# Kernel optimization log

Measured on AMD Instinct MI355X. Metric: run time of the kernel, lower is better.

The kernel has to match this reference:

```python
import jax, jax.numpy as jnp
import numpy as np

N = 6144      # total atoms
F = 128       # hidden_dim
NB = 48       # number of molecules (batch segments)
LONG_RANGE_SCALE = 1.0


def setup_inputs() -> dict:
    key = jax.random.key(0)
    ks = jax.random.split(key, 16)
    s = 1.0 / np.sqrt(F)
    return {
        "h0": jax.random.normal(ks[0], (N, F), jnp.float32),
        "h1": jax.random.normal(ks[1], (N, 3, F), jnp.float32),
        "pos": jax.random.normal(ks[2], (N, 3), jnp.float32),
        "batch": jnp.sort(jax.random.randint(ks[3], (N,), 0, NB)),
        "qW1": jax.random.normal(ks[4], (F, F // 2), jnp.float32) * s,
        "qb1": jnp.zeros((F // 2,), jnp.float32),
        "qW2": jax.random.normal(ks[5], (F // 2, 1), jnp.float32) * s,
        "qb2": jnp.zeros((1,), jnp.float32),
        "cW1": jax.random.normal(ks[6], (F, F // 2), jnp.float32) * s,
        "cb1": jnp.zeros((F // 2,), jnp.float32),
        "cW2": jax.random.normal(ks[7], (F // 2, 1), jnp.float32) * s,
        "cb2": jnp.zeros((1,), jnp.float32),
        "muW": jax.random.normal(ks[8], (F, 1), jnp.float32) * s,
    }


def reference(h0, h1, pos, batch, qW1, qb1, qW2, qb2, cW1, cb1, cW2, cb2, muW):
    n = pos.shape[0]
    # pairwise geometry
    batch_mask = batch[:, None] == batch[None, :]                 # (N,N) bool
    diff = pos[:, None, :] - pos[None, :, :]                      # (N,N,3)
    dist_sq = jnp.sum(diff * diff, axis=-1)                       # (N,N)
    dist = jnp.sqrt(dist_sq + 1e-8)
    valid = batch_mask & ~jnp.eye(n, dtype=bool)
    validf = valid.astype(dist.dtype)

    energy = jnp.zeros((), dist.dtype)

    # --- Coulomb (use_charge) ---
    q = jax.nn.silu(h0 @ qW1 + qb1) @ qW2 + qb2                   # (N,1)
    q_sum = jax.ops.segment_sum(q, batch, num_segments=NB)        # (NB,1)
    cnt = jax.ops.segment_sum(jnp.ones((n, 1), q.dtype), batch, num_segments=NB)
    q_mean = q_sum / jnp.maximum(cnt, 1.0)                        # scatter_mean
    q = q - q_mean[batch]                                         # per-molecule neutrality
    qq = q @ q.T                                                  # (N,N)
    f_taper = 1.0 - jnp.exp(-0.5 * dist)
    E_coul = jnp.sum(qq / dist * f_taper * validf)
    energy = energy + 0.5 * E_coul * 14.399

    # --- van der Waals (use_vdw) ---
    c6 = jax.nn.softplus(jax.nn.silu(h0 @ cW1 + cb1) @ cW2 + cb2)  # (N,1), >0
    c6_ij = jnp.sqrt(c6 @ c6.T)                                    # (N,N)
    r6 = dist_sq ** 3
    E_vdw = -jnp.sum(c6_ij / (r6 + 20.0) * validf)
    energy = energy + 0.5 * E_vdw

    # --- dipole-dipole (use_dipole) ---
    mu = (h1 @ muW)[..., 0]                                        # (N,3)
    mu_dot_mu = mu @ mu.T                                          # (N,N)
    n_ij = diff / (dist[..., None] + 1e-8)                         # (N,N,3)
    mu_dot_n_i = jnp.einsum("id,ijd->ij", mu, n_ij)
    mu_dot_n_j = jnp.einsum("jd,ijd->ij", mu, n_ij)
    inv_r3 = 1.0 / (dist_sq * dist + 10.0)
    E_dip = jnp.sum((mu_dot_mu - 3.0 * mu_dot_n_i * mu_dot_n_j) * inv_r3 * validf)
    energy = energy + 0.5 * E_dip

    return energy * LONG_RANGE_SCALE
```

## Files before the change

### kernel.cpp

```cpp
#include <hip/hip_runtime.h>
#include <math.h>

#define F 128
#define H 64
#define HH 32
#define AT 64
#define NBMOL 48
#define CAP 256
#define SPLIT 16

__device__ __forceinline__ float silu_f(float x) {
    return x / (1.0f + __expf(-x));
}
__device__ __forceinline__ float softplus_f(float x) {
    return fmaxf(x, 0.0f) + log1pf(__expf(-fabsf(x)));
}
__device__ __forceinline__ float frcp(float x) {
    return __builtin_amdgcn_rcpf(x);
}
__device__ __forceinline__ float dot4(float4 a, float4 b) {
    return fmaf(a.x, b.x, fmaf(a.y, b.y, fmaf(a.z, b.z, a.w * b.w)));
}

__global__ __launch_bounds__(256, 4) void k_atom(
    const float* __restrict__ h0, const float* __restrict__ h1,
    const int* __restrict__ batch,
    const float* __restrict__ qW1, const float* __restrict__ qb1,
    const float* __restrict__ qW2,
    const float* __restrict__ cW1, const float* __restrict__ cb1,
    const float* __restrict__ cW2,
    const float* __restrict__ muW,
    float* __restrict__ part,
    float* __restrict__ mu,
    int* __restrict__ segstart, int* __restrict__ segend,
    float* __restrict__ out, int N, int nmlp, int ndip)
{
    __shared__ float4 sW4[HH * 32];
    __shared__ float4 sX4[AT * 32];
    __shared__ float red[4][AT];

    const int b = blockIdx.x;
    const int tid = threadIdx.x;

    if (b < nmlp) {
        const int tile  = b >> 2;
        const int net   = b & 1;
        const int hhalf = (b >> 1) & 1;
        const float* __restrict__ W1 = net ? cW1 : qW1;
        const float* __restrict__ b1 = net ? cb1 : qb1;
        const float* __restrict__ W2 = net ? cW2 : qW2;

        for (int idx = tid; idx < HH * F; idx += 256) {
            int f = idx >> 5;
            int hh = idx & 31;
            float val = W1[f * H + hhalf * HH + hh];
            int f4 = f >> 2, fi = f & 3;
            ((float*)&sW4[hh * 32 + (f4 ^ ((hh >> 1) & 7))])[fi] = val;
        }
        const float4* __restrict__ h0v = (const float4*)h0;
        for (int idx = tid; idx < AT * 32; idx += 256) {
            int a = idx >> 5, f4 = idx & 31;
            int row = min(tile * AT + a, N - 1);
            sX4[a * 32 + (f4 ^ ((a >> 2) & 7))] = h0v[(size_t)row * 32 + f4];
        }
        __syncthreads();

        const int ag = tid & 15;
        const int hg = tid >> 4;
        const int swx = ag & 7;
        const int sww = hg & 7;
        const int h0i = hhalf * HH + 2 * hg;

        float z[4][2];
        {
            float b0 = b1[h0i], b1v = b1[h0i + 1];
            #pragma unroll
            for (int j = 0; j < 4; ++j) { z[j][0] = b0; z[j][1] = b1v; }
        }

        #pragma unroll 4
        for (int f4 = 0; f4 < 32; ++f4) {
            float4 w0 = sW4[(2 * hg) * 32 + (f4 ^ sww)];
            float4 w1 = sW4[(2 * hg + 1) * 32 + (f4 ^ sww)];
            #pragma unroll
            for (int j = 0; j < 4; ++j) {
                float4 x = sX4[(4 * ag + j) * 32 + (f4 ^ swx)];
                z[j][0] += dot4(x, w0);
                z[j][1] += dot4(x, w1);
            }
        }

        const float w2a = W2[h0i], w2b = W2[h0i + 1];
        float p[4];
        #pragma unroll
        for (int j = 0; j < 4; ++j)
            p[j] = fmaf(silu_f(z[j][0]), w2a, silu_f(z[j][1]) * w2b);

        #pragma unroll
        for (int j = 0; j < 4; ++j) {
            p[j] += __shfl_xor(p[j], 16);
            p[j] += __shfl_xor(p[j], 32);
        }
        const int wv = tid >> 6, lane = tid & 63;
        if (lane < 16) {
            #pragma unroll
            for (int j = 0; j < 4; ++j) red[wv][4 * lane + j] = p[j];
        }
        __syncthreads();
        if (tid < AT) {
            float s = red[0][tid] + red[1][tid] + red[2][tid] + red[3][tid];
            int atom = tile * AT + tid;
            if (atom < N) part[(size_t)(net * 2 + hhalf) * N + atom] = s;
        }
    } else if (b < nmlp + ndip) {
        const int slot = tid >> 4;
        const int l = tid & 15;
        int row = (b - nmlp) * 16 + slot;
        if (row < 3 * N) {
            const float4* rp = (const float4*)(h1 + (size_t)row * F);
            const float4* mp = (const float4*)muW;
            float pm = dot4(rp[2 * l], mp[2 * l]) +
                       dot4(rp[2 * l + 1], mp[2 * l + 1]);
            #pragma unroll
            for (int off = 1; off < 16; off <<= 1) pm += __shfl_xor(pm, off);
            if (l == 0) mu[row] = pm;
        }
    } else {
        if (tid == 0) out[0] = 0.0f;
        for (int i = tid; i < N; i += 256) {
            int bb = batch[i];
            if (i == 0 || batch[i - 1] != bb) segstart[bb] = i;
            if (i == N - 1 || batch[i + 1] != bb) segend[bb] = i + 1;
        }
    }
}

__global__ __launch_bounds__(256) void k_pair(
    const float* __restrict__ pos,
    const float* __restrict__ part,
    const float* __restrict__ mu,
    const float* __restrict__ qb2, const float* __restrict__ cb2,
    const int* __restrict__ segstart, const int* __restrict__ segend,
    float* __restrict__ out, int N)
{
    const int b = blockIdx.x;
    const int s = blockIdx.y;
    const int tid = threadIdx.x;
    const int st = segstart[b];
    const int n = segend[b] - st;

    const float* __restrict__ p0 = part;
    const float* __restrict__ p1 = part + N;
    const float* __restrict__ p2 = part + 2 * (size_t)N;
    const float* __restrict__ p3 = part + 3 * (size_t)N;
    const float qb2v = qb2[0], cb2v = cb2[0];

    __shared__ float sq[CAP], sc[CAP], sp[3 * CAP], sm[3 * CAP];
    __shared__ float red[4];

    float e_c = 0.f, e_v = 0.f, e_d = 0.f;

    if (n > 1 && n <= CAP) {
        float partsum = 0.f;
        for (int k = tid; k < n; k += 256) {
            float qv = p0[st + k] + p1[st + k] + qb2v;
            sq[k] = qv; partsum += qv;
            sc[k] = sqrtf(softplus_f(p2[st + k] + p3[st + k] + cb2v));
        }
        for (int k = tid; k < 3 * n; k += 256) {
            sp[k] = pos[3 * st + k];
            sm[k] = mu[3 * st + k];
        }
        #pragma unroll
        for (int off = 32; off > 0; off >>= 1)
            partsum += __shfl_xor(partsum, off);
        if ((tid & 63) == 0) red[tid >> 6] = partsum;
        __syncthreads();
        const float mean = (red[0] + red[1] + red[2] + red[3]) / (float)n;

        const int r = tid >> 4;
        const int c = tid & 15;
        for (int il = s + SPLIT * r; il < n; il += SPLIT * 16) {
            const float qi = sq[il] - mean;
            const float sci = sc[il];
            const float xi = sp[3 * il], yi = sp[3 * il + 1], zi = sp[3 * il + 2];
            const float mxi = sm[3 * il], myi = sm[3 * il + 1], mzi = sm[3 * il + 2];
            for (int jl = c; jl < n; jl += 16) {
                if (jl == il) continue;
                float dx = xi - sp[3 * jl], dy = yi - sp[3 * jl + 1],
                      dz = zi - sp[3 * jl + 2];
                float ds0 = fmaf(dx, dx, fmaf(dy, dy, dz * dz));
                float d = sqrtf(ds0 + 1e-8f);
                float inv_d = frcp(d);
                float qj = sq[jl] - mean;
                e_c = fmaf(qi * qj * inv_d, 1.0f - __expf(-0.5f * d), e_c);
                float r6 = ds0 * ds0 * ds0;
                e_v = fmaf(sci * sc[jl], frcp(r6 + 20.0f), e_v);
                float smx = sm[3 * jl], smy = sm[3 * jl + 1], smz = sm[3 * jl + 2];
                float mdm = fmaf(mxi, smx, fmaf(myi, smy, mzi * smz));
                float mdni = fmaf(mxi, dx, fmaf(myi, dy, mzi * dz)) * inv_d;
                float mdnj = fmaf(smx, dx, fmaf(smy, dy, smz * dz)) * inv_d;
                e_d = fmaf(mdm - 3.0f * mdni * mdnj,
                           frcp(fmaf(ds0, d, 10.0f)), e_d);
            }
        }
    } else if (n > CAP) {
        float partsum = 0.f;
        for (int k = tid; k < n; k += 256)
            partsum += p0[st + k] + p1[st + k] + qb2v;
        #pragma unroll
        for (int off = 32; off > 0; off >>= 1)
            partsum += __shfl_xor(partsum, off);
        if ((tid & 63) == 0) red[tid >> 6] = partsum;
        __syncthreads();
        const float mean = (red[0] + red[1] + red[2] + red[3]) / (float)n;
        const int r = tid >> 4, c = tid & 15;
        for (int j0 = 0; j0 < n; j0 += CAP) {
            const int chunk = min(CAP, n - j0);
            __syncthreads();
            for (int k = tid; k < chunk; k += 256) {
                int j = st + j0 + k;
                sq[k] = p0[j] + p1[j] + qb2v;
                sc[k] = sqrtf(softplus_f(p2[j] + p3[j] + cb2v));
            }
            for (int k = tid; k < 3 * chunk; k += 256) {
                sp[k] = pos[3 * (st + j0) + k];
                sm[k] = mu[3 * (st + j0) + k];
            }
            __syncthreads();
            for (int il = s + SPLIT * r; il < n; il += SPLIT * 16) {
                const int i = st + il;
                const float qi = p0[i] + p1[i] + qb2v - mean;
                const float sci = sqrtf(softplus_f(p2[i] + p3[i] + cb2v));
                const float xi = pos[i * 3], yi = pos[i * 3 + 1], zi = pos[i * 3 + 2];
                const float mxi = mu[i * 3], myi = mu[i * 3 + 1], mzi = mu[i * 3 + 2];
                for (int jl = c; jl < chunk; jl += 16) {
                    if (j0 + jl == il) continue;
                    float dx = xi - sp[3 * jl], dy = yi - sp[3 * jl + 1],
                          dz = zi - sp[3 * jl + 2];
                    float ds0 = fmaf(dx, dx, fmaf(dy, dy, dz * dz));
                    float d = sqrtf(ds0 + 1e-8f);
                    float inv_d = frcp(d);
                    float qj = sq[jl] - mean;
                    e_c = fmaf(qi * qj * inv_d, 1.0f - __expf(-0.5f * d), e_c);
                    float r6 = ds0 * ds0 * ds0;
                    e_v = fmaf(sci * sc[jl], frcp(r6 + 20.0f), e_v);
                    float smx = sm[3 * jl], smy = sm[3 * jl + 1], smz = sm[3 * jl + 2];
                    float mdm = fmaf(mxi, smx, fmaf(myi, smy, mzi * smz));
                    float mdni = fmaf(mxi, dx, fmaf(myi, dy, mzi * dz)) * inv_d;
                    float mdnj = fmaf(smx, dx, fmaf(smy, dy, smz * dz)) * inv_d;
                    e_d = fmaf(mdm - 3.0f * mdni * mdnj,
                               frcp(fmaf(ds0, d, 10.0f)), e_d);
                }
            }
        }
    }

    float vv = fmaf(7.1995f, e_c, fmaf(-0.5f, e_v, 0.5f * e_d));
    #pragma unroll
    for (int off = 32; off > 0; off >>= 1) vv += __shfl_xor(vv, off);
    __syncthreads();
    if ((tid & 63) == 0) red[tid >> 6] = vv;
    __syncthreads();
    if (tid == 0) atomicAdd(out, red[0] + red[1] + red[2] + red[3]);
}

extern "C" void kernel_launch(void* const* d_in, const int* in_sizes, int n_in,
                              void* d_out, int out_size, void* d_ws, size_t ws_size,
                              hipStream_t stream) {
    const float* h0  = (const float*)d_in[0];
    const float* h1  = (const float*)d_in[1];
    const float* pos = (const float*)d_in[2];
    const int*   batch = (const int*)d_in[3];
    const float* qW1 = (const float*)d_in[4];
    const float* qb1 = (const float*)d_in[5];
    const float* qW2 = (const float*)d_in[6];
    const float* qb2 = (const float*)d_in[7];
    const float* cW1 = (const float*)d_in[8];
    const float* cb1 = (const float*)d_in[9];
    const float* cW2 = (const float*)d_in[10];
    const float* cb2 = (const float*)d_in[11];
    const float* muW = (const float*)d_in[12];
    float* out = (float*)d_out;
    const int N = in_sizes[0] / F;

    float* ws = (float*)d_ws;
    int* segstart = (int*)ws;
    int* segend   = (int*)(ws + 48);
    float* part = ws + 128;
    float* mu   = part + 4 * (size_t)N;

    const int ntile = (N + AT - 1) / AT;
    const int nmlp = 4 * ntile;
    const int ndip = (3 * N + 15) / 16;
    const int grid = nmlp + ndip + 1;

    k_atom<<<grid, 256, 0, stream>>>(h0, h1, batch, qW1, qb1, qW2,
                                     cW1, cb1, cW2, muW,
                                     part, mu, segstart, segend, out,
                                     N, nmlp, ndip);
    k_pair<<<dim3(NBMOL, SPLIT), 256, 0, stream>>>(pos, part, mu, qb2, cb2,
                                                   segstart, segend, out, N);
}
```

Measured before the change: 112.5 us.

## Compute full hidden width per MLP block and fuse charge/C6 epilogue into atom kernel

Result: no change. 111.9 us (-0.5%).

```diff
diff --git a/kernel.cpp b/kernel.cpp
--- a/kernel.cpp
+++ b/kernel.cpp
@@ -3,8 +3,7 @@
 
 #define F 128
 #define H 64
-#define HH 32
-#define AT 64
+#define ATILE 32
 #define NBMOL 48
 #define CAP 256
 #define SPLIT 16
@@ -26,62 +25,61 @@
     const float* __restrict__ h0, const float* __restrict__ h1,
     const int* __restrict__ batch,
     const float* __restrict__ qW1, const float* __restrict__ qb1,
-    const float* __restrict__ qW2,
+    const float* __restrict__ qW2, const float* __restrict__ qb2,
     const float* __restrict__ cW1, const float* __restrict__ cb1,
-    const float* __restrict__ cW2,
+    const float* __restrict__ cW2, const float* __restrict__ cb2,
     const float* __restrict__ muW,
-    float* __restrict__ part,
+    float* __restrict__ qout,
+    float* __restrict__ sqc6,
     float* __restrict__ mu,
     int* __restrict__ segstart, int* __restrict__ segend,
     float* __restrict__ out, int N, int nmlp, int ndip)
 {
-    __shared__ float4 sW4[HH * 32];
-    __shared__ float4 sX4[AT * 32];
-    __shared__ float red[4][AT];
+    __shared__ float4 sW4[H * 32];
+    __shared__ float4 sX4[ATILE * 32];
+    __shared__ float red[4][ATILE];
 
     const int b = blockIdx.x;
     const int tid = threadIdx.x;
 
     if (b < nmlp) {
-        const int tile  = b >> 2;
-        const int net   = b & 1;
-        const int hhalf = (b >> 1) & 1;
+        const int tile = b >> 1;
+        const int net  = b & 1;
         const float* __restrict__ W1 = net ? cW1 : qW1;
         const float* __restrict__ b1 = net ? cb1 : qb1;
         const float* __restrict__ W2 = net ? cW2 : qW2;
 
-        for (int idx = tid; idx < HH * F; idx += 256) {
-            int f = idx >> 5;
-            int hh = idx & 31;
-            float val = W1[f * H + hhalf * HH + hh];
+        for (int idx = tid; idx < H * F; idx += 256) {
+            int f = idx >> 6, h = idx & 63;
+            float val = W1[idx];
             int f4 = f >> 2, fi = f & 3;
-            ((float*)&sW4[hh * 32 + (f4 ^ ((hh >> 1) & 7))])[fi] = val;
+            ((float*)&sW4[h * 32 + (f4 ^ ((h >> 1) & 7))])[fi] = val;
         }
         const float4* __restrict__ h0v = (const float4*)h0;
-        for (int idx = tid; idx < AT * 32; idx += 256) {
+        for (int idx = tid; idx < ATILE * 32; idx += 256) {
             int a = idx >> 5, f4 = idx & 31;
-            int row = min(tile * AT + a, N - 1);
+            int row = min(tile * ATILE + a, N - 1);
             sX4[a * 32 + (f4 ^ ((a >> 2) & 7))] = h0v[(size_t)row * 32 + f4];
         }
         __syncthreads();
 
-        const int ag = tid & 15;
-        const int hg = tid >> 4;
-        const int swx = ag & 7;
+        const int ag = tid & 7;
+        const int hg = tid >> 3;
+        const int swx = ag;
         const int sww = hg & 7;
-        const int h0i = hhalf * HH + 2 * hg;
+        const int h0i = 2 * hg;
 
         float z[4][2];
         {
-            float b0 = b1[h0i], b1v = b1[h0i + 1];
+            float c0 = b1[h0i], c1 = b1[h0i + 1];
             #pragma unroll
-            for (int j = 0; j < 4; ++j) { z[j][0] = b0; z[j][1] = b1v; }
+            for (int j = 0; j < 4; ++j) { z[j][0] = c0; z[j][1] = c1; }
         }
 
         #pragma unroll 4
         for (int f4 = 0; f4 < 32; ++f4) {
-            float4 w0 = sW4[(2 * hg) * 32 + (f4 ^ sww)];
-            float4 w1 = sW4[(2 * hg + 1) * 32 + (f4 ^ sww)];
+            float4 w0 = sW4[h0i * 32 + (f4 ^ sww)];
+            float4 w1 = sW4[(h0i + 1) * 32 + (f4 ^ sww)];
             #pragma unroll
             for (int j = 0; j < 4; ++j) {
                 float4 x = sX4[(4 * ag + j) * 32 + (f4 ^ swx)];
@@ -98,32 +96,41 @@
 
         #pragma unroll
         for (int j = 0; j < 4; ++j) {
+            p[j] += __shfl_xor(p[j], 8);
             p[j] += __shfl_xor(p[j], 16);
             p[j] += __shfl_xor(p[j], 32);
         }
         const int wv = tid >> 6, lane = tid & 63;
-        if (lane < 16) {
+        if (lane < 8) {
             #pragma unroll
             for (int j = 0; j < 4; ++j) red[wv][4 * lane + j] = p[j];
         }
         __syncthreads();
-        if (tid < AT) {
+        if (tid < ATILE) {
             float s = red[0][tid] + red[1][tid] + red[2][tid] + red[3][tid];
-            int atom = tile * AT + tid;
-            if (atom < N) part[(size_t)(net * 2 + hhalf) * N + atom] = s;
+            int atom = tile * ATILE + tid;
+            if (atom < N) {
+                if (net == 0) qout[atom] = s + qb2[0];
+                else          sqc6[atom] = sqrtf(softplus_f(s + cb2[0]));
+            }
         }
     } else if (b < nmlp + ndip) {
         const int slot = tid >> 4;
         const int l = tid & 15;
-        int row = (b - nmlp) * 16 + slot;
-        if (row < 3 * N) {
-            const float4* rp = (const float4*)(h1 + (size_t)row * F);
-            const float4* mp = (const float4*)muW;
-            float pm = dot4(rp[2 * l], mp[2 * l]) +
-                       dot4(rp[2 * l + 1], mp[2 * l + 1]);
-            #pragma unroll
-            for (int off = 1; off < 16; off <<= 1) pm += __shfl_xor(pm, off);
-            if (l == 0) mu[row] = pm;
+        const float4* mp = (const float4*)muW;
+        const float4 m0 = mp[2 * l];
+        const float4 m1 = mp[2 * l + 1];
+        const int base = (b - nmlp) * 64;
+        #pragma unroll
+        for (int rr = 0; rr < 4; ++rr) {
+            int row = base + slot + 16 * rr;
+            if (row < 3 * N) {
+                const float4* rp = (const float4*)(h1 + (size_t)row * F);
+                float pm = dot4(rp[2 * l], m0) + dot4(rp[2 * l + 1], m1);
+                #pragma unroll
+                for (int off = 1; off < 16; off <<= 1) pm += __shfl_xor(pm, off);
+                if (l == 0) mu[row] = pm;
+            }
         }
     } else {
         if (tid == 0) out[0] = 0.0f;
@@ -137,9 +144,9 @@
 
 __global__ __launch_bounds__(256) void k_pair(
     const float* __restrict__ pos,
-    const float* __restrict__ part,
+    const float* __restrict__ qg,
+    const float* __restrict__ cg,
     const float* __restrict__ mu,
-    const float* __restrict__ qb2, const float* __restrict__ cb2,
     const int* __restrict__ segstart, const int* __restrict__ segend,
     float* __restrict__ out, int N)
 {
@@ -149,12 +156,6 @@
     const int st = segstart[b];
     const int n = segend[b] - st;
 
-    const float* __restrict__ p0 = part;
-    const float* __restrict__ p1 = part + N;
-    const float* __restrict__ p2 = part + 2 * (size_t)N;
-    const float* __restrict__ p3 = part + 3 * (size_t)N;
-    const float qb2v = qb2[0], cb2v = cb2[0];
-
     __shared__ float sq[CAP], sc[CAP], sp[3 * CAP], sm[3 * CAP];
     __shared__ float red[4];
 
@@ -163,9 +164,9 @@
     if (n > 1 && n <= CAP) {
         float partsum = 0.f;
         for (int k = tid; k < n; k += 256) {
-            float qv = p0[st + k] + p1[st + k] + qb2v;
+            float qv = qg[st + k];
             sq[k] = qv; partsum += qv;
-            sc[k] = sqrtf(softplus_f(p2[st + k] + p3[st + k] + cb2v));
+            sc[k] = cg[st + k];
         }
         for (int k = tid; k < 3 * n; k += 256) {
             sp[k] = pos[3 * st + k];
@@ -177,11 +178,13 @@
         if ((tid & 63) == 0) red[tid >> 6] = partsum;
         __syncthreads();
         const float mean = (red[0] + red[1] + red[2] + red[3]) / (float)n;
+        for (int k = tid; k < n; k += 256) sq[k] -= mean;
+        __syncthreads();
 
         const int r = tid >> 4;
         const int c = tid & 15;
         for (int il = s + SPLIT * r; il < n; il += SPLIT * 16) {
-            const float qi = sq[il] - mean;
+            const float qi = sq[il];
             const float sci = sc[il];
             const float xi = sp[3 * il], yi = sp[3 * il + 1], zi = sp[3 * il + 2];
             const float mxi = sm[3 * il], myi = sm[3 * il + 1], mzi = sm[3 * il + 2];
@@ -192,7 +195,7 @@
                 float ds0 = fmaf(dx, dx, fmaf(dy, dy, dz * dz));
                 float d = sqrtf(ds0 + 1e-8f);
                 float inv_d = frcp(d);
-                float qj = sq[jl] - mean;
+                float qj = sq[jl];
                 e_c = fmaf(qi * qj * inv_d, 1.0f - __expf(-0.5f * d), e_c);
                 float r6 = ds0 * ds0 * ds0;
                 e_v = fmaf(sci * sc[jl], frcp(r6 + 20.0f), e_v);
@@ -207,7 +210,7 @@
     } else if (n > CAP) {
         float partsum = 0.f;
         for (int k = tid; k < n; k += 256)
-            partsum += p0[st + k] + p1[st + k] + qb2v;
+            partsum += qg[st + k];
         #pragma unroll
         for (int off = 32; off > 0; off >>= 1)
             partsum += __shfl_xor(partsum, off);
@@ -220,8 +223,8 @@
             __syncthreads();
             for (int k = tid; k < chunk; k += 256) {
                 int j = st + j0 + k;
-                sq[k] = p0[j] + p1[j] + qb2v;
-                sc[k] = sqrtf(softplus_f(p2[j] + p3[j] + cb2v));
+                sq[k] = qg[j] - mean;
+                sc[k] = cg[j];
             }
             for (int k = tid; k < 3 * chunk; k += 256) {
                 sp[k] = pos[3 * (st + j0) + k];
@@ -230,8 +233,8 @@
             __syncthreads();
             for (int il = s + SPLIT * r; il < n; il += SPLIT * 16) {
                 const int i = st + il;
-                const float qi = p0[i] + p1[i] + qb2v - mean;
-                const float sci = sqrtf(softplus_f(p2[i] + p3[i] + cb2v));
+                const float qi = qg[i] - mean;
+                const float sci = cg[i];
                 const float xi = pos[i * 3], yi = pos[i * 3 + 1], zi = pos[i * 3 + 2];
                 const float mxi = mu[i * 3], myi = mu[i * 3 + 1], mzi = mu[i * 3 + 2];
                 for (int jl = c; jl < chunk; jl += 16) {
@@ -241,7 +244,7 @@
                     float ds0 = fmaf(dx, dx, fmaf(dy, dy, dz * dz));
                     float d = sqrtf(ds0 + 1e-8f);
                     float inv_d = frcp(d);
-                    float qj = sq[jl] - mean;
+                    float qj = sq[jl];
                     e_c = fmaf(qi * qj * inv_d, 1.0f - __expf(-0.5f * d), e_c);
                     float r6 = ds0 * ds0 * ds0;
                     e_v = fmaf(sci * sc[jl], frcp(r6 + 20.0f), e_v);
@@ -287,18 +290,20 @@
     float* ws = (float*)d_ws;
     int* segstart = (int*)ws;
     int* segend   = (int*)(ws + 48);
-    float* part = ws + 128;
-    float* mu   = part + 4 * (size_t)N;
-
-    const int ntile = (N + AT - 1) / AT;
-    const int nmlp = 4 * ntile;
-    const int ndip = (3 * N + 15) / 16;
+    float* qplane = ws + 128;
+    float* cplane = qplane + (size_t)N;
+    float* mu     = cplane + (size_t)N;
+
+    const int ntile = (N + ATILE - 1) / ATILE;
+    const int nmlp = 2 * ntile;
+    const int ndip = (3 * N + 63) / 64;
     const int grid = nmlp + ndip + 1;
 
-    k_atom<<<grid, 256, 0, stream>>>(h0, h1, batch, qW1, qb1, qW2,
-                                     cW1, cb1, cW2, muW,
-                                     part, mu, segstart, segend, out,
+    k_atom<<<grid, 256, 0, stream>>>(h0, h1, batch,
+                                     qW1, qb1, qW2, qb2,
+                                     cW1, cb1, cW2, cb2, muW,
+                                     qplane, cplane, mu, segstart, segend, out,
                                      N, nmlp, ndip);
-    k_pair<<<dim3(NBMOL, SPLIT), 256, 0, stream>>>(pos, part, mu, qb2, cb2,
+    k_pair<<<dim3(NBMOL, SPLIT), 256, 0, stream>>>(pos, qplane, cplane, mu,
                                                    segstart, segend, out, N);
 }
```
